# Kernel tuning notes

Measured on AMD Instinct MI355X. Metric: run time of the kernel, lower is better.

The kernel has to match this reference:

```python
import jax, jax.numpy as jnp
import numpy as np

N_NODES = 100000
N_EDGES = 1600000
D_FEAT = 64


def setup_inputs() -> dict:
    key = jax.random.key(0)
    k1, k2, k3 = jax.random.split(key, 3)
    adj_indices = jax.random.randint(k1, (2, N_EDGES), 0, N_NODES, dtype=jnp.int64 if jax.config.jax_enable_x64 else jnp.int32)
    # symmetric-normalized-like edge weights in (0, 1)
    adj_values = jax.random.uniform(k2, (N_EDGES,), dtype=jnp.float32)
    feats = jax.random.normal(k3, (N_NODES, D_FEAT), dtype=jnp.float32)
    return {"adj_indices": adj_indices, "adj_values": adj_values, "feats": feats}


def reference(adj_indices, adj_values, feats):
    """out = sparse_adj @ feats  (COO SpMM via gather + segment_sum).

    adj_indices: [2, E] int (row, col) coordinates of nonzeros
    adj_values : [E] float nonzero values
    feats      : [N, d] dense node features
    returns    : [N, d]
    """
    rows = adj_indices[0]
    cols = adj_indices[1]
    # gather neighbor features, scale by edge weight: [E, d]
    msgs = adj_values[:, None] * feats[cols]
    # scatter-add into destination rows: [N, d]
    return jax.ops.segment_sum(msgs, rows, num_segments=feats.shape[0])
```

## Files before the change

kernel.cpp:

```cpp
#include <hip/hip_runtime.h>

#define NN 100000
#define NE 1600000
#define DF 64
#define RPB 32
#define NBS 3328
#define NBU 3125
#define OFS_STRIDE (NBS + 1)
#define CHK 4096
#define NC 391
#define CVTB 1024
#define CVT_N (NN * DF / 8)
#define SCAP 768
#define SPB 13

__device__ inline float bflo(unsigned int u) { return __uint_as_float(u << 16); }
__device__ inline float bfhi(unsigned int u) { return __uint_as_float(u & 0xFFFF0000u); }

__device__ inline unsigned int bfpack(float lo, float hi) {
    unsigned int ul = __float_as_uint(lo), uh = __float_as_uint(hi);
    ul = (ul + 0x7FFFu + ((ul >> 16) & 1u)) >> 16;
    uh = (uh + 0x7FFFu + ((uh >> 16) & 1u)) & 0xFFFF0000u;
    return ul | uh;
}

__global__ __launch_bounds__(256) void prep_kernel(
    const int* __restrict__ rows, const int* __restrict__ cols,
    const float* __restrict__ vals, const float* __restrict__ feats,
    unsigned short* __restrict__ ofs, int2* __restrict__ packed,
    uint4* __restrict__ fbf, int E)
{
    __shared__ int cnt[NBS];
    __shared__ int scanv[NBS];
    __shared__ int tsum[256];

    int t = threadIdx.x;

    if (blockIdx.x >= NC) {
        const float4* f4 = reinterpret_cast<const float4*>(feats);
        for (int idx = (blockIdx.x - NC) * 256 + t; idx < CVT_N; idx += CVTB * 256) {
            float4 a = f4[2 * idx];
            float4 b = f4[2 * idx + 1];
            uint4 o;
            o.x = bfpack(a.x, a.y);
            o.y = bfpack(a.z, a.w);
            o.z = bfpack(b.x, b.y);
            o.w = bfpack(b.z, b.w);
            fbf[idx] = o;
        }
        return;
    }

    int c = blockIdx.x;
    int base = c * CHK;
    int n = E - base; if (n > CHK) n = CHK;

    for (int b = t; b < NBS; b += 256) cnt[b] = 0;
    __syncthreads();

    int rr[16]; int cc[16]; float vv[16];
#pragma unroll
    for (int k = 0; k < 16; ++k) {
        int i = t + k * 256;
        if (i < n) {
            rr[k] = rows[base + i];
            cc[k] = cols[base + i];
            vv[k] = vals[base + i];
            atomicAdd(&cnt[rr[k] >> 5], 1);
        }
    }
    __syncthreads();

    int local[SPB]; int s = 0;
#pragma unroll
    for (int j = 0; j < SPB; ++j) { local[j] = cnt[t * SPB + j]; s += local[j]; }
    tsum[t] = s;
    __syncthreads();
    for (int d = 1; d < 256; d <<= 1) {
        int x = (t >= d) ? tsum[t - d] : 0;
        __syncthreads();
        tsum[t] += x;
        __syncthreads();
    }
    int run = tsum[t] - s;
#pragma unroll
    for (int j = 0; j < SPB; ++j) { scanv[t * SPB + j] = run; run += local[j]; }
    __syncthreads();

    unsigned short* og = ofs + (size_t)c * OFS_STRIDE;
    for (int b = t; b < NBS; b += 256) og[b] = (unsigned short)scanv[b];
    if (t == 0) og[NBS] = (unsigned short)n;
    __syncthreads();

#pragma unroll
    for (int k = 0; k < 16; ++k) {
        int i = t + k * 256;
        if (i < n) {
            int r = rr[k];
            int pos = base + atomicAdd(&scanv[r >> 5], 1);
            packed[pos] = make_int2(cc[k] | ((r & 31) << 17), __float_as_int(vv[k]));
        }
    }
}

__global__ __launch_bounds__(256) void spmm_kernel(
    const unsigned short* __restrict__ ofs, const int2* __restrict__ packed,
    const unsigned short* __restrict__ fbf, float* __restrict__ out, int nc)
{
    int borig = blockIdx.x;
    int xcd = borig & 7;
    int sub = borig >> 3;
    int b = (xcd < 5 ? xcd * 391 : 5 * 391 + (xcd - 5) * 390) + sub;

    int t = threadIdx.x;

    __shared__ int2 sorted[SCAP];
    __shared__ int cnt[RPB];
    __shared__ int rstart[RPB + 1];

    if (t < RPB) cnt[t] = 0;
    __syncthreads();

    int c2 = t + 256;
    int sA = 0, eA = 0, sB = 0, eB = 0;
    if (t < nc) {
        const unsigned short* og = ofs + (size_t)t * OFS_STRIDE + b;
        sA = og[0]; eA = og[1];
    }
    if (c2 < nc) {
        const unsigned short* og = ofs + (size_t)c2 * OFS_STRIDE + b;
        sB = og[0]; eB = og[1];
    }
    int lenA = eA - sA, lenB = eB - sB;

    int2 ebA[8], ebB[8];
#pragma unroll
    for (int k = 0; k < 8; ++k) if (k < lenA) ebA[k] = packed[t * CHK + sA + k];
#pragma unroll
    for (int k = 0; k < 8; ++k) if (k < lenB) ebB[k] = packed[c2 * CHK + sB + k];

#pragma unroll
    for (int k = 0; k < 8; ++k) if (k < lenA) atomicAdd(&cnt[(ebA[k].x >> 17) & 31], 1);
    for (int i = sA + 8; i < eA; ++i) atomicAdd(&cnt[(packed[t * CHK + i].x >> 17) & 31], 1);
#pragma unroll
    for (int k = 0; k < 8; ++k) if (k < lenB) atomicAdd(&cnt[(ebB[k].x >> 17) & 31], 1);
    for (int i = sB + 8; i < eB; ++i) atomicAdd(&cnt[(packed[c2 * CHK + i].x >> 17) & 31], 1);
    __syncthreads();

    if (t < RPB) {
        int v = cnt[t];
        int incl = v;
        for (int d = 1; d < RPB; d <<= 1) {
            int x = __shfl_up(incl, d, 64);
            if (t >= d) incl += x;
        }
        rstart[t] = incl - v;
        if (t == RPB - 1) rstart[RPB] = incl;
    }
    __syncthreads();
    if (t < RPB) cnt[t] = rstart[t];
    __syncthreads();

#pragma unroll
    for (int k = 0; k < 8; ++k) if (k < lenA) {
        int rl = (ebA[k].x >> 17) & 31;
        int pos = atomicAdd(&cnt[rl], 1);
        if (pos < SCAP) sorted[pos] = make_int2(ebA[k].x & 0x1FFFF, ebA[k].y);
    }
    for (int i = sA + 8; i < eA; ++i) {
        int2 cv = packed[t * CHK + i];
        int rl = (cv.x >> 17) & 31;
        int pos = atomicAdd(&cnt[rl], 1);
        if (pos < SCAP) sorted[pos] = make_int2(cv.x & 0x1FFFF, cv.y);
    }
#pragma unroll
    for (int k = 0; k < 8; ++k) if (k < lenB) {
        int rl = (ebB[k].x >> 17) & 31;
        int pos = atomicAdd(&cnt[rl], 1);
        if (pos < SCAP) sorted[pos] = make_int2(ebB[k].x & 0x1FFFF, ebB[k].y);
    }
    for (int i = sB + 8; i < eB; ++i) {
        int2 cv = packed[c2 * CHK + i];
        int rl = (cv.x >> 17) & 31;
        int pos = atomicAdd(&cnt[rl], 1);
        if (pos < SCAP) sorted[pos] = make_int2(cv.x & 0x1FFFF, cv.y);
    }
    __syncthreads();

    int w = t >> 6;
    int lane = t & 63;
    int grp = lane >> 4;
    int fq = lane & 15;
    int rowbase = b * RPB;

    for (int rl = w * 8; rl < w * 8 + 8; ++rl) {
        int row = rowbase + rl;
        int beg = rstart[rl], end = rstart[rl + 1];
        float4 acc = make_float4(0.f, 0.f, 0.f, 0.f);
        int i = beg + grp;
        for (; i + 12 < end; i += 16) {
            int2 e0 = sorted[i];
            int2 e1 = sorted[i + 4];
            int2 e2 = sorted[i + 8];
            int2 e3 = sorted[i + 12];
            const uint2 g0 = *reinterpret_cast<const uint2*>(fbf + (size_t)e0.x * DF + fq * 4);
            const uint2 g1 = *reinterpret_cast<const uint2*>(fbf + (size_t)e1.x * DF + fq * 4);
            const uint2 g2 = *reinterpret_cast<const uint2*>(fbf + (size_t)e2.x * DF + fq * 4);
            const uint2 g3 = *reinterpret_cast<const uint2*>(fbf + (size_t)e3.x * DF + fq * 4);
            float v0 = __int_as_float(e0.y), v1 = __int_as_float(e1.y);
            float v2 = __int_as_float(e2.y), v3 = __int_as_float(e3.y);
            acc.x += v0 * bflo(g0.x); acc.y += v0 * bfhi(g0.x);
            acc.z += v0 * bflo(g0.y); acc.w += v0 * bfhi(g0.y);
            acc.x += v1 * bflo(g1.x); acc.y += v1 * bfhi(g1.x);
            acc.z += v1 * bflo(g1.y); acc.w += v1 * bfhi(g1.y);
            acc.x += v2 * bflo(g2.x); acc.y += v2 * bfhi(g2.x);
            acc.z += v2 * bflo(g2.y); acc.w += v2 * bfhi(g2.y);
            acc.x += v3 * bflo(g3.x); acc.y += v3 * bfhi(g3.x);
            acc.z += v3 * bflo(g3.y); acc.w += v3 * bfhi(g3.y);
        }
        for (; i + 4 < end; i += 8) {
            int2 e0 = sorted[i];
            int2 e1 = sorted[i + 4];
            const uint2 g0 = *reinterpret_cast<const uint2*>(fbf + (size_t)e0.x * DF + fq * 4);
            const uint2 g1 = *reinterpret_cast<const uint2*>(fbf + (size_t)e1.x * DF + fq * 4);
            float v0 = __int_as_float(e0.y), v1 = __int_as_float(e1.y);
            acc.x += v0 * bflo(g0.x); acc.y += v0 * bfhi(g0.x);
            acc.z += v0 * bflo(g0.y); acc.w += v0 * bfhi(g0.y);
            acc.x += v1 * bflo(g1.x); acc.y += v1 * bfhi(g1.x);
            acc.z += v1 * bflo(g1.y); acc.w += v1 * bfhi(g1.y);
        }
        if (i < end) {
            int2 e0 = sorted[i];
            const uint2 g0 = *reinterpret_cast<const uint2*>(fbf + (size_t)e0.x * DF + fq * 4);
            float v0 = __int_as_float(e0.y);
            acc.x += v0 * bflo(g0.x); acc.y += v0 * bfhi(g0.x);
            acc.z += v0 * bflo(g0.y); acc.w += v0 * bfhi(g0.y);
        }
#pragma unroll
        for (int m = 16; m <= 32; m <<= 1) {
            acc.x += __shfl_xor(acc.x, m, 64);
            acc.y += __shfl_xor(acc.y, m, 64);
            acc.z += __shfl_xor(acc.z, m, 64);
            acc.w += __shfl_xor(acc.w, m, 64);
        }
        if (grp == 0)
            *reinterpret_cast<float4*>(out + (size_t)row * DF + fq * 4) = acc;
    }
}


extern "C" void kernel_launch(void* const* d_in, const int* in_sizes, int n_in,
                              void* d_out, int out_size, void* d_ws, size_t ws_size,
                              hipStream_t stream) {
    const int* adj_indices = (const int*)d_in[0];
    const float* adj_values = (const float*)d_in[1];
    const float* feats = (const float*)d_in[2];
    float* out = (float*)d_out;

    const int E = in_sizes[1];
    const int* rows = adj_indices;
    const int* cols = adj_indices + E;

    unsigned short* fbf = (unsigned short*)d_ws;
    size_t fbf_bytes = (size_t)NN * DF * 2;
    unsigned short* ofs = (unsigned short*)((char*)d_ws + fbf_bytes);
    size_t ofs_bytes = (size_t)NC * OFS_STRIDE * 2;
    size_t packed_off = (fbf_bytes + ofs_bytes + 15) & ~(size_t)15;
    int2* packed = (int2*)((char*)d_ws + packed_off);

    prep_kernel<<<NC + CVTB, 256, 0, stream>>>(rows, cols, adj_values, feats,
                                               ofs, packed, (uint4*)fbf, E);
    spmm_kernel<<<NBU, 256, 0, stream>>>(ofs, packed, fbf, out, NC);
}
```

Before: 65.24 us.

## Split SpMM into merge-to-global-CSR kernel plus per-row gather kernel

Replaces the fused per-block merge+gather SpMM with two stages: a merge kernel that sorts each 32-row bucket's edges and writes them to a global sorted array with per-row metadata, then a separate gather kernel with one wavefront per row and more blocks. The aim is to decouple the latency-bound merge from the gather so the gather runs at higher occupancy with unrolled independent loads. It adds an extra write and read of the full edge list, a memset, and an extra launch. The new path is used only if the workspace is large enough.

Result: slower. 114.1 us (+74.9%).

```diff
diff --git a/kernel.cpp b/kernel.cpp
--- a/kernel.cpp
+++ b/kernel.cpp
@@ -13,6 +13,7 @@
 #define CVT_N (NN * DF / 8)
 #define SCAP 768
 #define SPB 13
+#define K3B 25000
 
 __device__ inline float bflo(unsigned int u) { return __uint_as_float(u << 16); }
 __device__ inline float bfhi(unsigned int u) { return __uint_as_float(u & 0xFFFF0000u); }
@@ -101,6 +102,172 @@
             packed[pos] = make_int2(cc[k] | ((r & 31) << 17), __float_as_int(vv[k]));
         }
     }
+}
+
+__global__ __launch_bounds__(256) void merge_kernel(
+    const unsigned short* __restrict__ ofs, const int2* __restrict__ packed,
+    int2* __restrict__ sortedg, int2* __restrict__ rowmeta,
+    int* __restrict__ gcur, int nc)
+{
+    int borig = blockIdx.x;
+    int xcd = borig & 7;
+    int sub = borig >> 3;
+    int b = (xcd < 5 ? xcd * 391 : 5 * 391 + (xcd - 5) * 390) + sub;
+
+    int t = threadIdx.x;
+
+    __shared__ int2 sorted[SCAP];
+    __shared__ int cnt[RPB];
+    __shared__ int rstart[RPB + 1];
+    __shared__ int sbase;
+
+    if (t < RPB) cnt[t] = 0;
+    __syncthreads();
+
+    int c2 = t + 256;
+    int sA = 0, eA = 0, sB = 0, eB = 0;
+    if (t < nc) {
+        const unsigned short* og = ofs + (size_t)t * OFS_STRIDE + b;
+        sA = og[0]; eA = og[1];
+    }
+    if (c2 < nc) {
+        const unsigned short* og = ofs + (size_t)c2 * OFS_STRIDE + b;
+        sB = og[0]; eB = og[1];
+    }
+    int lenA = eA - sA, lenB = eB - sB;
+
+    int2 ebA[8], ebB[8];
+#pragma unroll
+    for (int k = 0; k < 8; ++k) if (k < lenA) ebA[k] = packed[t * CHK + sA + k];
+#pragma unroll
+    for (int k = 0; k < 8; ++k) if (k < lenB) ebB[k] = packed[c2 * CHK + sB + k];
+
+#pragma unroll
+    for (int k = 0; k < 8; ++k) if (k < lenA) atomicAdd(&cnt[(ebA[k].x >> 17) & 31], 1);
+    for (int i = sA + 8; i < eA; ++i) atomicAdd(&cnt[(packed[t * CHK + i].x >> 17) & 31], 1);
+#pragma unroll
+    for (int k = 0; k < 8; ++k) if (k < lenB) atomicAdd(&cnt[(ebB[k].x >> 17) & 31], 1);
+    for (int i = sB + 8; i < eB; ++i) atomicAdd(&cnt[(packed[c2 * CHK + i].x >> 17) & 31], 1);
+    __syncthreads();
+
+    if (t < RPB) {
+        int v = cnt[t];
+        int incl = v;
+        for (int d = 1; d < RPB; d <<= 1) {
+            int x = __shfl_up(incl, d, 64);
+            if (t >= d) incl += x;
+        }
+        rstart[t] = incl - v;
+        if (t == RPB - 1) rstart[RPB] = incl;
+    }
+    __syncthreads();
+    if (t < RPB) cnt[t] = rstart[t];
+    __syncthreads();
+
+#pragma unroll
+    for (int k = 0; k < 8; ++k) if (k < lenA) {
+        int rl = (ebA[k].x >> 17) & 31;
+        int pos = atomicAdd(&cnt[rl], 1);
+        if (pos < SCAP) sorted[pos] = make_int2(ebA[k].x & 0x1FFFF, ebA[k].y);
+    }
+    for (int i = sA + 8; i < eA; ++i) {
+        int2 cv = packed[t * CHK + i];
+        int rl = (cv.x >> 17) & 31;
+        int pos = atomicAdd(&cnt[rl], 1);
+        if (pos < SCAP) sorted[pos] = make_int2(cv.x & 0x1FFFF, cv.y);
+    }
+#pragma unroll
+    for (int k = 0; k < 8; ++k) if (k < lenB) {
+        int rl = (ebB[k].x >> 17) & 31;
+        int pos = atomicAdd(&cnt[rl], 1);
+        if (pos < SCAP) sorted[pos] = make_int2(ebB[k].x & 0x1FFFF, ebB[k].y);
+    }
+    for (int i = sB + 8; i < eB; ++i) {
+        int2 cv = packed[c2 * CHK + i];
+        int rl = (cv.x >> 17) & 31;
+        int pos = atomicAdd(&cnt[rl], 1);
+        if (pos < SCAP) sorted[pos] = make_int2(cv.x & 0x1FFFF, cv.y);
+    }
+    __syncthreads();
+
+    int total = rstart[RPB]; if (total > SCAP) total = SCAP;
+    if (t == 0) sbase = atomicAdd(gcur, total);
+    __syncthreads();
+    int base0 = sbase;
+    if (t < RPB) {
+        int st = rstart[t] < SCAP ? rstart[t] : SCAP;
+        int en = rstart[t + 1] < SCAP ? rstart[t + 1] : SCAP;
+        rowmeta[b * RPB + t] = make_int2(base0 + st, en - st);
+    }
+    for (int i = t; i < total; i += 256) sortedg[base0 + i] = sorted[i];
+}
+
+__global__ __launch_bounds__(256) void spmm3_kernel(
+    const int2* __restrict__ rowmeta, const int2* __restrict__ sortedg,
+    const unsigned short* __restrict__ fbf, float* __restrict__ out)
+{
+    int bid = blockIdx.x;
+    int b = (bid & 7) * 3125 + (bid >> 3);
+
+    int t = threadIdx.x;
+    int w = t >> 6;
+    int lane = t & 63;
+    int grp = lane >> 4;
+    int fq = lane & 15;
+
+    int row = b * 4 + w;
+    int2 meta = rowmeta[row];
+    int start = meta.x, end = meta.x + meta.y;
+
+    float4 acc = make_float4(0.f, 0.f, 0.f, 0.f);
+    int i = start + grp;
+    for (; i + 12 < end; i += 16) {
+        int2 e0 = sortedg[i];
+        int2 e1 = sortedg[i + 4];
+        int2 e2 = sortedg[i + 8];
+        int2 e3 = sortedg[i + 12];
+        const uint2 g0 = *reinterpret_cast<const uint2*>(fbf + (size_t)e0.x * DF + fq * 4);
+        const uint2 g1 = *reinterpret_cast<const uint2*>(fbf + (size_t)e1.x * DF + fq * 4);
+        const uint2 g2 = *reinterpret_cast<const uint2*>(fbf + (size_t)e2.x * DF + fq * 4);
+        const uint2 g3 = *reinterpret_cast<const uint2*>(fbf + (size_t)e3.x * DF + fq * 4);
+        float v0 = __int_as_float(e0.y), v1 = __int_as_float(e1.y);
+        float v2 = __int_as_float(e2.y), v3 = __int_as_float(e3.y);
+        acc.x += v0 * bflo(g0.x); acc.y += v0 * bfhi(g0.x);
+        acc.z += v0 * bflo(g0.y); acc.w += v0 * bfhi(g0.y);
+        acc.x += v1 * bflo(g1.x); acc.y += v1 * bfhi(g1.x);
+        acc.z += v1 * bflo(g1.y); acc.w += v1 * bfhi(g1.y);
+        acc.x += v2 * bflo(g2.x); acc.y += v2 * bfhi(g2.x);
+        acc.z += v2 * bflo(g2.y); acc.w += v2 * bfhi(g2.y);
+        acc.x += v3 * bflo(g3.x); acc.y += v3 * bfhi(g3.x);
+        acc.z += v3 * bflo(g3.y); acc.w += v3 * bfhi(g3.y);
+    }
+    for (; i + 4 < end; i += 8) {
+        int2 e0 = sortedg[i];
+        int2 e1 = sortedg[i + 4];
+        const uint2 g0 = *reinterpret_cast<const uint2*>(fbf + (size_t)e0.x * DF + fq * 4);
+        const uint2 g1 = *reinterpret_cast<const uint2*>(fbf + (size_t)e1.x * DF + fq * 4);
+        float v0 = __int_as_float(e0.y), v1 = __int_as_float(e1.y);
+        acc.x += v0 * bflo(g0.x); acc.y += v0 * bfhi(g0.x);
+        acc.z += v0 * bflo(g0.y); acc.w += v0 * bfhi(g0.y);
+        acc.x += v1 * bflo(g1.x); acc.y += v1 * bfhi(g1.x);
+        acc.z += v1 * bflo(g1.y); acc.w += v1 * bfhi(g1.y);
+    }
+    if (i < end) {
+        int2 e0 = sortedg[i];
+        const uint2 g0 = *reinterpret_cast<const uint2*>(fbf + (size_t)e0.x * DF + fq * 4);
+        float v0 = __int_as_float(e0.y);
+        acc.x += v0 * bflo(g0.x); acc.y += v0 * bfhi(g0.x);
+        acc.z += v0 * bflo(g0.y); acc.w += v0 * bfhi(g0.y);
+    }
+#pragma unroll
+    for (int m = 16; m <= 32; m <<= 1) {
+        acc.x += __shfl_xor(acc.x, m, 64);
+        acc.y += __shfl_xor(acc.y, m, 64);
+        acc.z += __shfl_xor(acc.z, m, 64);
+        acc.w += __shfl_xor(acc.w, m, 64);
+    }
+    if (grp == 0)
+        *reinterpret_cast<float4*>(out + (size_t)row * DF + fq * 4) = acc;
 }
 
 __global__ __launch_bounds__(256) void spmm_kernel(
@@ -261,14 +428,24 @@
     const int* rows = adj_indices;
     const int* cols = adj_indices + E;
 
-    unsigned short* fbf = (unsigned short*)d_ws;
-    size_t fbf_bytes = (size_t)NN * DF * 2;
-    unsigned short* ofs = (unsigned short*)((char*)d_ws + fbf_bytes);
-    size_t ofs_bytes = (size_t)NC * OFS_STRIDE * 2;
-    size_t packed_off = (fbf_bytes + ofs_bytes + 15) & ~(size_t)15;
-    int2* packed = (int2*)((char*)d_ws + packed_off);
+    char* ws = (char*)d_ws;
+    size_t off = 0;
+    unsigned short* fbf = (unsigned short*)(ws + off); off += (size_t)NN * DF * 2;
+    unsigned short* ofs = (unsigned short*)(ws + off); off += (size_t)NC * OFS_STRIDE * 2;
+    off = (off + 15) & ~(size_t)15;
+    int2* packed = (int2*)(ws + off); off += (size_t)NE * 8;
+    int2* sortedg = (int2*)(ws + off); off += (size_t)NE * 8;
+    int2* rowmeta = (int2*)(ws + off); off += (size_t)NN * 8;
+    int* gcur = (int*)(ws + off); off += 64;
+    const bool big = (ws_size >= off);
 
     prep_kernel<<<NC + CVTB, 256, 0, stream>>>(rows, cols, adj_values, feats,
                                                ofs, packed, (uint4*)fbf, E);
-    spmm_kernel<<<NBU, 256, 0, stream>>>(ofs, packed, fbf, out, NC);
-}
+    if (big) {
+        hipMemsetAsync(gcur, 0, sizeof(int), stream);
+        merge_kernel<<<NBU, 256, 0, stream>>>(ofs, packed, sortedg, rowmeta, gcur, NC);
+        spmm3_kernel<<<K3B, 256, 0, stream>>>(rowmeta, sortedg, fbf, out);
+    } else {
+        spmm_kernel<<<NBU, 256, 0, stream>>>(ofs, packed, fbf, out, NC);
+    }
+}
```
